# Optimization experiments

Measured on AMD Instinct MI355X. Metric: run time of the kernel, lower is better.

The kernel has to match this reference:

```python
import jax, jax.numpy as jnp
import numpy as np

EPS = 1e-6
K_HOPS = 2  # SGConv K


def setup_inputs() -> dict:
    key = jax.random.key(0)
    k1, k2, k3, k4 = jax.random.split(key, 4)
    B, Kk, C, T = 32, 8, 64, 250
    E, H = 4096, 128
    x = jax.random.normal(k1, (B, Kk, C, T), dtype=jnp.float32)
    edge_index = jax.random.randint(k2, (2, E), 0, C, dtype=jnp.int64)
    edge_weights = jax.random.uniform(k3, (E,), dtype=jnp.float32)
    W = jax.random.normal(k4, (H, Kk * T), dtype=jnp.float32) * 0.02
    b = jnp.zeros((H,), dtype=jnp.float32)
    return {"x": x, "edge_index": edge_index, "edge_weights": edge_weights, "W": W, "b": b}


def reference(x, edge_index, edge_weights, W, b):
    B, Kk, C, T = x.shape
    N = C  # nodes
    x = x.reshape(B, N, Kk * T)  # (B, N, F)

    # clamp non-positive edge weights to epsilon (mirrors in-place .data clamp)
    w = jnp.where(edge_weights <= 0, EPS, edge_weights)

    # gcn_norm with self loops (fill value 1.0)
    src, dst = edge_index[0], edge_index[1]
    loop = jnp.arange(N, dtype=edge_index.dtype)
    src = jnp.concatenate([src, loop])
    dst = jnp.concatenate([dst, loop])
    w = jnp.concatenate([w, jnp.ones((N,), w.dtype)])
    deg = jnp.zeros((N,), w.dtype).at[dst].add(w)
    dinv = jnp.where(deg > 0, deg ** -0.5, jnp.zeros_like(deg))
    norm = dinv[src] * w * dinv[dst]  # (E+N,)

    # K hops of gather -> weight -> scatter-add aggregation
    for _ in range(K_HOPS):
        msg = x[:, src, :] * norm[None, :, None]        # (B, E+N, F)
        x = jnp.zeros_like(x).at[:, dst, :].add(msg)    # (B, N, F)

    # final linear: y = x @ W^T + b
    return jnp.einsum('bnf,hf->bnh', x, W) + b
```

## Files before the change

kernel.cpp:

```cpp
#include <hip/hip_runtime.h>
#include <hip/hip_bf16.h>

#define EPSW 1e-6f

typedef __attribute__((ext_vector_type(4))) float floatx4;
typedef __attribute__((ext_vector_type(8))) short shortx8;

__device__ __forceinline__ unsigned short f2bf(float f) {
    unsigned int u = __float_as_uint(f);
    u = (u + 0x7fffu + ((u >> 16) & 1u)) >> 16;
    return (unsigned short)u;
}

__global__ __launch_bounds__(256) void prep(const float* __restrict__ x,
                                            const float* __restrict__ W,
                                            const int* __restrict__ ei,
                                            const float* __restrict__ ew,
                                            unsigned short* __restrict__ xt,
                                            unsigned short* __restrict__ wt,
                                            float* __restrict__ Mt) {
    __shared__ __align__(16) unsigned char smem[64 * 264 * 2];
    const int bid = blockIdx.x;
    const int t   = threadIdx.x;

    if (bid < 256) {
        unsigned short(*tile)[264] = (unsigned short(*)[264])smem;
        const int rb   = (bid >> 3) * 64;
        const int kgb  = (bid & 7) * 32;
        const int kbas = kgb * 8;
#pragma unroll
        for (int i = 0; i < 16; ++i) {
            const int idx = i * 256 + t;
            const int r   = idx >> 6;
            const int kc  = (idx & 63) * 4;
            const int k   = kbas + kc;
            floatx4 v = (floatx4){0.f, 0.f, 0.f, 0.f};
            if (k < 2000)
                v = *(const floatx4*)(x + (size_t)(rb + r) * 2000 + k);
            tile[r][kc + 0] = f2bf(v.x);
            tile[r][kc + 1] = f2bf(v.y);
            tile[r][kc + 2] = f2bf(v.z);
            tile[r][kc + 3] = f2bf(v.w);
        }
        __syncthreads();
#pragma unroll
        for (int i = 0; i < 8; ++i) {
            const int kg_l = i * 4 + (t >> 6);
            const int r    = t & 63;
            const shortx8 g = *(const shortx8*)&tile[r][kg_l * 8];
            *(shortx8*)(xt + ((size_t)(kgb + kg_l) * 2048 + rb + r) * 8) = g;
        }
    } else if (bid < 272) {
#pragma unroll
        for (int i = 0; i < 8; ++i) {
            const int G  = (bid - 256) * 2048 + i * 256 + t;
            const int kg = G >> 7;
            const int h  = G & 127;
            const int k  = kg * 8;
            floatx4 v0 = (floatx4){0.f, 0.f, 0.f, 0.f};
            floatx4 v1 = (floatx4){0.f, 0.f, 0.f, 0.f};
            if (k < 2000) {
                v0 = *(const floatx4*)(W + (size_t)h * 2000 + k);
                v1 = *(const floatx4*)(W + (size_t)h * 2000 + k + 4);
            }
            unsigned short* p = wt + ((size_t)kg * 128 + h) * 8;
            p[0] = f2bf(v0.x); p[1] = f2bf(v0.y); p[2] = f2bf(v0.z); p[3] = f2bf(v0.w);
            p[4] = f2bf(v1.x); p[5] = f2bf(v1.y); p[6] = f2bf(v1.z); p[7] = f2bf(v1.w);
        }
    } else {
        float* A    = (float*)smem;
        float* deg  = (float*)(smem + 16384);
        float* dinv = deg + 64;
        if (t < 64) deg[t] = 1.0f;
        for (int i = t; i < 4096; i += 256) A[i] = 0.0f;
        __syncthreads();
        const int* src = ei;
        const int* dst = ei + 4096;
        for (int e = t; e < 4096; e += 256) {
            float w = ew[e];
            w = (w <= 0.0f) ? EPSW : w;
            atomicAdd(&deg[dst[e]], w);
        }
        __syncthreads();
        if (t < 64) dinv[t] = 1.0f / sqrtf(deg[t]);
        __syncthreads();
        for (int e = t; e < 4096; e += 256) {
            float w = ew[e];
            w = (w <= 0.0f) ? EPSW : w;
            const int s = src[e], d = dst[e];
            atomicAdd(&A[d * 64 + s], dinv[s] * w * dinv[d]);
        }
        if (t < 64) atomicAdd(&A[t * 64 + t], dinv[t] * dinv[t]);
        __syncthreads();
#pragma unroll
        for (int i = 0; i < 16; ++i) {
            const int idx = i * 256 + t;
            const int n = idx >> 6, c = idx & 63;
            float s = 0.0f;
#pragma unroll 8
            for (int k = 0; k < 64; ++k) s += A[n * 64 + k] * A[k * 64 + c];
            Mt[c * 64 + n] = s;
        }
    }
}

__global__ __launch_bounds__(256) void gemm(const unsigned short* __restrict__ xt,
                                            const unsigned short* __restrict__ wt,
                                            float* __restrict__ z) {
    const int t    = threadIdx.x;
    const int wave = t >> 6, lane = t & 63;
    const int m = lane & 15, q = lane >> 4;
    const int rbase = blockIdx.x * 16;
    const int hbase = blockIdx.y * 64 + wave * 16;

    const shortx8* Ag = (const shortx8*)xt;
    const shortx8* Bg = (const shortx8*)wt;
    int ga = q * 2048 + rbase + m;
    int gb = q * 128 + hbase + m;

    floatx4 acc0 = (floatx4){0.f, 0.f, 0.f, 0.f};
    floatx4 acc1 = (floatx4){0.f, 0.f, 0.f, 0.f};
#pragma unroll 4
    for (int kt = 0; kt < 64; kt += 2) {
        const shortx8 a0 = Ag[ga];
        const shortx8 b0 = Bg[gb];
        const shortx8 a1 = Ag[ga + 8192];
        const shortx8 b1 = Bg[gb + 512];
        acc0 = __builtin_amdgcn_mfma_f32_16x16x32_bf16(a0, b0, acc0, 0, 0, 0);
        acc1 = __builtin_amdgcn_mfma_f32_16x16x32_bf16(a1, b1, acc1, 0, 0, 0);
        ga += 16384; gb += 1024;
    }
#pragma unroll
    for (int v = 0; v < 4; ++v)
        z[(size_t)(rbase + q * 4 + v) * 128 + hbase + m] = acc0[v] + acc1[v];
}

__global__ __launch_bounds__(256) void apply_M(const float* __restrict__ z,
                                               const float* __restrict__ Mtg,
                                               const float* __restrict__ bias,
                                               float* __restrict__ y) {
    __shared__ float Ms[4096];
    __shared__ float zs[64][16];
    const int b  = blockIdx.x;
    const int hc = blockIdx.y;
    const int t  = threadIdx.x;
#pragma unroll
    for (int i = 0; i < 16; ++i) Ms[i * 256 + t] = Mtg[i * 256 + t];
#pragma unroll
    for (int i = 0; i < 4; ++i) {
        const int idx = i * 256 + t;
        const int mr = idx >> 4, hh = idx & 15;
        zs[mr][hh] = z[(size_t)(b * 64 + mr) * 128 + hc * 16 + hh];
    }
    __syncthreads();
    const int h  = t & 15;
    const int n0 = (t >> 4) * 4;
    const float bv = bias[hc * 16 + h];
    float s0 = bv, s1 = bv, s2 = bv, s3 = bv;
#pragma unroll
    for (int mm = 0; mm < 64; ++mm) {
        const float zv = zs[mm][h];
        s0 += Ms[mm * 64 + n0 + 0] * zv;
        s1 += Ms[mm * 64 + n0 + 1] * zv;
        s2 += Ms[mm * 64 + n0 + 2] * zv;
        s3 += Ms[mm * 64 + n0 + 3] * zv;
    }
    float* yp = y + (size_t)b * 8192 + (size_t)n0 * 128 + hc * 16 + h;
    yp[0]   = s0;
    yp[128] = s1;
    yp[256] = s2;
    yp[384] = s3;
}

extern "C" void kernel_launch(void* const* d_in, const int* in_sizes, int n_in,
                              void* d_out, int out_size, void* d_ws, size_t ws_size,
                              hipStream_t stream) {
    const float* x    = (const float*)d_in[0];
    const int*   ei   = (const int*)d_in[1];
    const float* ew   = (const float*)d_in[2];
    const float* W    = (const float*)d_in[3];
    const float* bias = (const float*)d_in[4];
    float* y = (float*)d_out;

    float* z  = (float*)d_ws;
    float* Mt = z + 262144;
    unsigned short* xt = (unsigned short*)(Mt + 4096);
    unsigned short* wt = xt + 4194304;

    prep<<<273, 256, 0, stream>>>(x, W, ei, ew, xt, wt, Mt);
    gemm<<<dim3(128, 2), 256, 0, stream>>>(xt, wt, z);
    apply_M<<<dim3(32, 8), 256, 0, stream>>>(z, Mt, bias, y);
}
```

Before: 103.4 us.

## Fuse x bf16 conversion into GEMM, reading fp32 x directly

Drops the prep pass that converted x to bf16 and rearranged it into a k-grouped layout in a workspace. The GEMM now loads fp32 rows of x directly, packs them to bf16 in registers with byte permutes, and feeds MFMA. This removes a full write and re-read of a 16 MB bf16 copy of x. In exchange the GEMM reads fp32 (twice the bytes per element), does strided per-row loads, rounds to bf16 with a simpler rounding rule, and splits the K loop into 63 dependent steps with boundary checks.

```diff
diff --git a/kernel.cpp b/kernel.cpp
--- a/kernel.cpp
+++ b/kernel.cpp
@@ -12,48 +12,30 @@
     return (unsigned short)u;
 }
 
-__global__ __launch_bounds__(256) void prep(const float* __restrict__ x,
-                                            const float* __restrict__ W,
-                                            const int* __restrict__ ei,
-                                            const float* __restrict__ ew,
-                                            unsigned short* __restrict__ xt,
-                                            unsigned short* __restrict__ wt,
-                                            float* __restrict__ Mt) {
-    __shared__ __align__(16) unsigned char smem[64 * 264 * 2];
+__device__ __forceinline__ shortx8 pack8(floatx4 a, floatx4 b) {
+    union { shortx8 v; unsigned int u[4]; } r;
+    const unsigned a0 = __float_as_uint(a.x) + 0x8000u, a1 = __float_as_uint(a.y) + 0x8000u;
+    const unsigned a2 = __float_as_uint(a.z) + 0x8000u, a3 = __float_as_uint(a.w) + 0x8000u;
+    const unsigned b0 = __float_as_uint(b.x) + 0x8000u, b1 = __float_as_uint(b.y) + 0x8000u;
+    const unsigned b2 = __float_as_uint(b.z) + 0x8000u, b3 = __float_as_uint(b.w) + 0x8000u;
+    r.u[0] = __builtin_amdgcn_perm(a1, a0, 0x07060302u);
+    r.u[1] = __builtin_amdgcn_perm(a3, a2, 0x07060302u);
+    r.u[2] = __builtin_amdgcn_perm(b1, b0, 0x07060302u);
+    r.u[3] = __builtin_amdgcn_perm(b3, b2, 0x07060302u);
+    return r.v;
+}
+
+__global__ __launch_bounds__(256) void prep_small(const float* __restrict__ W,
+                                                  const int* __restrict__ ei,
+                                                  const float* __restrict__ ew,
+                                                  unsigned short* __restrict__ wt,
+                                                  float* __restrict__ Mt) {
     const int bid = blockIdx.x;
     const int t   = threadIdx.x;
-
-    if (bid < 256) {
-        unsigned short(*tile)[264] = (unsigned short(*)[264])smem;
-        const int rb   = (bid >> 3) * 64;
-        const int kgb  = (bid & 7) * 32;
-        const int kbas = kgb * 8;
+    if (bid < 32) {
 #pragma unroll
-        for (int i = 0; i < 16; ++i) {
-            const int idx = i * 256 + t;
-            const int r   = idx >> 6;
-            const int kc  = (idx & 63) * 4;
-            const int k   = kbas + kc;
-            floatx4 v = (floatx4){0.f, 0.f, 0.f, 0.f};
-            if (k < 2000)
-                v = *(const floatx4*)(x + (size_t)(rb + r) * 2000 + k);
-            tile[r][kc + 0] = f2bf(v.x);
-            tile[r][kc + 1] = f2bf(v.y);
-            tile[r][kc + 2] = f2bf(v.z);
-            tile[r][kc + 3] = f2bf(v.w);
-        }
-        __syncthreads();
-#pragma unroll
-        for (int i = 0; i < 8; ++i) {
-            const int kg_l = i * 4 + (t >> 6);
-            const int r    = t & 63;
-            const shortx8 g = *(const shortx8*)&tile[r][kg_l * 8];
-            *(shortx8*)(xt + ((size_t)(kgb + kg_l) * 2048 + rb + r) * 8) = g;
-        }
-    } else if (bid < 272) {
-#pragma unroll
-        for (int i = 0; i < 8; ++i) {
-            const int G  = (bid - 256) * 2048 + i * 256 + t;
+        for (int i = 0; i < 4; ++i) {
+            const int G  = bid * 1024 + i * 256 + t;
             const int kg = G >> 7;
             const int h  = G & 127;
             const int k  = kg * 8;
@@ -68,9 +50,9 @@
             p[4] = f2bf(v1.x); p[5] = f2bf(v1.y); p[6] = f2bf(v1.z); p[7] = f2bf(v1.w);
         }
     } else {
-        float* A    = (float*)smem;
-        float* deg  = (float*)(smem + 16384);
-        float* dinv = deg + 64;
+        __shared__ float A[4096];
+        __shared__ float deg[64];
+        __shared__ float dinv[64];
         if (t < 64) deg[t] = 1.0f;
         for (int i = t; i < 4096; i += 256) A[i] = 0.0f;
         __syncthreads();
@@ -104,35 +86,36 @@
     }
 }
 
-__global__ __launch_bounds__(256) void gemm(const unsigned short* __restrict__ xt,
-                                            const unsigned short* __restrict__ wt,
-                                            float* __restrict__ z) {
+__global__ __launch_bounds__(256) void gemm_direct(const float* __restrict__ x,
+                                                   const unsigned short* __restrict__ wt,
+                                                   float* __restrict__ z) {
     const int t    = threadIdx.x;
     const int wave = t >> 6, lane = t & 63;
     const int m = lane & 15, q = lane >> 4;
-    const int rbase = blockIdx.x * 16;
-    const int hbase = blockIdx.y * 64 + wave * 16;
-
-    const shortx8* Ag = (const shortx8*)xt;
+    const int b  = blockIdx.y;
+    const int rt = blockIdx.x >> 1, hh = blockIdx.x & 1;
+    const float* xrow = x + (size_t)(b * 64 + rt * 16 + m) * 2000;
+    const int htile = hh * 4 + wave;
     const shortx8* Bg = (const shortx8*)wt;
-    int ga = q * 2048 + rbase + m;
-    int gb = q * 128 + hbase + m;
+    const int gb = q * 128 + htile * 16 + m;
 
     floatx4 acc0 = (floatx4){0.f, 0.f, 0.f, 0.f};
     floatx4 acc1 = (floatx4){0.f, 0.f, 0.f, 0.f};
-#pragma unroll 4
-    for (int kt = 0; kt < 64; kt += 2) {
-        const shortx8 a0 = Ag[ga];
-        const shortx8 b0 = Bg[gb];
-        const shortx8 a1 = Ag[ga + 8192];
-        const shortx8 b1 = Bg[gb + 512];
-        acc0 = __builtin_amdgcn_mfma_f32_16x16x32_bf16(a0, b0, acc0, 0, 0, 0);
-        acc1 = __builtin_amdgcn_mfma_f32_16x16x32_bf16(a1, b1, acc1, 0, 0, 0);
-        ga += 16384; gb += 1024;
+#pragma unroll 9
+    for (int s = 0; s < 63; ++s) {
+        const int k0 = s * 32 + q * 8;
+        floatx4 f0 = (floatx4){0.f, 0.f, 0.f, 0.f};
+        floatx4 f1 = (floatx4){0.f, 0.f, 0.f, 0.f};
+        if (k0 < 2000)     f0 = *(const floatx4*)(xrow + k0);
+        if (k0 + 4 < 2000) f1 = *(const floatx4*)(xrow + k0 + 4);
+        const shortx8 af = pack8(f0, f1);
+        const shortx8 bf = Bg[gb + s * 512];
+        if (s & 1) acc1 = __builtin_amdgcn_mfma_f32_16x16x32_bf16(af, bf, acc1, 0, 0, 0);
+        else       acc0 = __builtin_amdgcn_mfma_f32_16x16x32_bf16(af, bf, acc0, 0, 0, 0);
     }
 #pragma unroll
     for (int v = 0; v < 4; ++v)
-        z[(size_t)(rbase + q * 4 + v) * 128 + hbase + m] = acc0[v] + acc1[v];
+        z[(size_t)(b * 64 + rt * 16 + q * 4 + v) * 128 + htile * 16 + m] = acc0[v] + acc1[v];
 }
 
 __global__ __launch_bounds__(256) void apply_M(const float* __restrict__ z,
@@ -184,10 +167,9 @@
 
     float* z  = (float*)d_ws;
     float* Mt = z + 262144;
-    unsigned short* xt = (unsigned short*)(Mt + 4096);
-    unsigned short* wt = xt + 4194304;
+    unsigned short* wt = (unsigned short*)(Mt + 4096);
 
-    prep<<<273, 256, 0, stream>>>(x, W, ei, ew, xt, wt, Mt);
-    gemm<<<dim3(128, 2), 256, 0, stream>>>(xt, wt, z);
+    prep_small<<<33, 256, 0, stream>>>(W, ei, ew, wt, Mt);
+    gemm_direct<<<dim3(8, 32), 256, 0, stream>>>(x, wt, z);
     apply_M<<<dim3(32, 8), 256, 0, stream>>>(z, Mt, bias, y);
 }
```

After: 117.0 us. +13.1%, slower.

## Fuse prep, GEMM and apply_M into one cooperative kernel with grid syncs

Applied to the files above, without the earlier changes.

Merges the three launches into a single cooperative kernel of 256 blocks, separating the phases with grid-wide syncs. The W conversion is spread across blocks, and the adjacency/M computation is folded onto the last block after its x tile. The intent is to remove launch gaps and tail effects between kernels. In exchange it adds grid-sync overhead and puts the serial M build on one block's critical path before the first sync.

```diff
diff --git a/kernel.cpp b/kernel.cpp
--- a/kernel.cpp
+++ b/kernel.cpp
@@ -1,5 +1,8 @@
 #include <hip/hip_runtime.h>
 #include <hip/hip_bf16.h>
+#include <hip/hip_cooperative_groups.h>
+
+namespace cg = cooperative_groups;
 
 #define EPSW 1e-6f
 
@@ -12,18 +15,18 @@
     return (unsigned short)u;
 }
 
-__global__ __launch_bounds__(256) void prep(const float* __restrict__ x,
-                                            const float* __restrict__ W,
-                                            const int* __restrict__ ei,
-                                            const float* __restrict__ ew,
-                                            unsigned short* __restrict__ xt,
-                                            unsigned short* __restrict__ wt,
-                                            float* __restrict__ Mt) {
-    __shared__ __align__(16) unsigned char smem[64 * 264 * 2];
+__global__ __launch_bounds__(256) void fused(
+        const float* __restrict__ x, const float* __restrict__ W,
+        const int* __restrict__ ei, const float* __restrict__ ew,
+        const float* __restrict__ bias,
+        unsigned short* __restrict__ xt, unsigned short* __restrict__ wt,
+        float* __restrict__ Mt, float* __restrict__ z, float* __restrict__ y) {
+    __shared__ __align__(16) unsigned char smem[50688];
     const int bid = blockIdx.x;
     const int t   = threadIdx.x;
+    cg::grid_group grid = cg::this_grid();
 
-    if (bid < 256) {
+    {
         unsigned short(*tile)[264] = (unsigned short(*)[264])smem;
         const int rb   = (bid >> 3) * 64;
         const int kgb  = (bid & 7) * 32;
@@ -42,21 +45,8 @@
             tile[r][kc + 2] = f2bf(v.z);
             tile[r][kc + 3] = f2bf(v.w);
         }
-        __syncthreads();
-#pragma unroll
-        for (int i = 0; i < 8; ++i) {
-            const int kg_l = i * 4 + (t >> 6);
-            const int r    = t & 63;
-            const shortx8 g = *(const shortx8*)&tile[r][kg_l * 8];
-            *(shortx8*)(xt + ((size_t)(kgb + kg_l) * 2048 + rb + r) * 8) = g;
-        }
-    } else if (bid < 272) {
-#pragma unroll
-        for (int i = 0; i < 8; ++i) {
-            const int G  = (bid - 256) * 2048 + i * 256 + t;
-            const int kg = G >> 7;
-            const int h  = G & 127;
-            const int k  = kg * 8;
+        if (t < 128) {
+            const int kg = bid, h = t, k = kg * 8;
             floatx4 v0 = (floatx4){0.f, 0.f, 0.f, 0.f};
             floatx4 v1 = (floatx4){0.f, 0.f, 0.f, 0.f};
             if (k < 2000) {
@@ -67,109 +57,111 @@
             p[0] = f2bf(v0.x); p[1] = f2bf(v0.y); p[2] = f2bf(v0.z); p[3] = f2bf(v0.w);
             p[4] = f2bf(v1.x); p[5] = f2bf(v1.y); p[6] = f2bf(v1.z); p[7] = f2bf(v1.w);
         }
-    } else {
-        float* A    = (float*)smem;
-        float* deg  = (float*)(smem + 16384);
-        float* dinv = deg + 64;
-        if (t < 64) deg[t] = 1.0f;
-        for (int i = t; i < 4096; i += 256) A[i] = 0.0f;
         __syncthreads();
-        const int* src = ei;
-        const int* dst = ei + 4096;
-        for (int e = t; e < 4096; e += 256) {
-            float w = ew[e];
-            w = (w <= 0.0f) ? EPSW : w;
-            atomicAdd(&deg[dst[e]], w);
+#pragma unroll
+        for (int i = 0; i < 8; ++i) {
+            const int kg_l = i * 4 + (t >> 6);
+            const int r    = t & 63;
+            const shortx8 g = *(const shortx8*)&tile[r][kg_l * 8];
+            *(shortx8*)(xt + ((size_t)(kgb + kg_l) * 2048 + rb + r) * 8) = g;
+        }
+        if (bid == 255) {
+            float* A    = (float*)(smem + 33792);
+            float* deg  = A + 4096;
+            float* dinv = deg + 64;
+            if (t < 64) deg[t] = 1.0f;
+            for (int i = t; i < 4096; i += 256) A[i] = 0.0f;
+            __syncthreads();
+            const int* src = ei;
+            const int* dst = ei + 4096;
+            for (int e = t; e < 4096; e += 256) {
+                float w = ew[e];
+                w = (w <= 0.0f) ? EPSW : w;
+                atomicAdd(&deg[dst[e]], w);
+            }
+            __syncthreads();
+            if (t < 64) dinv[t] = 1.0f / sqrtf(deg[t]);
+            __syncthreads();
+            for (int e = t; e < 4096; e += 256) {
+                float w = ew[e];
+                w = (w <= 0.0f) ? EPSW : w;
+                const int s = src[e], d = dst[e];
+                atomicAdd(&A[d * 64 + s], dinv[s] * w * dinv[d]);
+            }
+            if (t < 64) atomicAdd(&A[t * 64 + t], dinv[t] * dinv[t]);
+            __syncthreads();
+#pragma unroll
+            for (int i = 0; i < 16; ++i) {
+                const int idx = i * 256 + t;
+                const int n = idx >> 6, c = idx & 63;
+                float s = 0.0f;
+#pragma unroll 8
+                for (int k = 0; k < 64; ++k) s += A[n * 64 + k] * A[k * 64 + c];
+                Mt[c * 64 + n] = s;
+            }
+        }
+    }
+    grid.sync();
+
+    {
+        const int wave = t >> 6, lane = t & 63;
+        const int m = lane & 15, q = lane >> 4;
+        const int rbase = (bid >> 1) * 16;
+        const int hbase = (bid & 1) * 64 + wave * 16;
+        const shortx8* Ag = (const shortx8*)xt;
+        const shortx8* Bg = (const shortx8*)wt;
+        int ga = q * 2048 + rbase + m;
+        int gb = q * 128 + hbase + m;
+        floatx4 acc0 = (floatx4){0.f, 0.f, 0.f, 0.f};
+        floatx4 acc1 = (floatx4){0.f, 0.f, 0.f, 0.f};
+#pragma unroll 4
+        for (int kt = 0; kt < 64; kt += 2) {
+            const shortx8 a0 = Ag[ga];
+            const shortx8 b0 = Bg[gb];
+            const shortx8 a1 = Ag[ga + 8192];
+            const shortx8 b1 = Bg[gb + 512];
+            acc0 = __builtin_amdgcn_mfma_f32_16x16x32_bf16(a0, b0, acc0, 0, 0, 0);
+            acc1 = __builtin_amdgcn_mfma_f32_16x16x32_bf16(a1, b1, acc1, 0, 0, 0);
+            ga += 16384; gb += 1024;
+        }
+#pragma unroll
+        for (int v = 0; v < 4; ++v)
+            z[(size_t)(rbase + q * 4 + v) * 128 + hbase + m] = acc0[v] + acc1[v];
+    }
+    grid.sync();
+
+    {
+        float* Ms       = (float*)smem;
+        float(*zs)[16]  = (float(*)[16])(smem + 16384);
+        const int b  = bid >> 3;
+        const int hc = bid & 7;
+#pragma unroll
+        for (int i = 0; i < 16; ++i) Ms[i * 256 + t] = Mt[i * 256 + t];
+#pragma unroll
+        for (int i = 0; i < 4; ++i) {
+            const int idx = i * 256 + t;
+            const int mr = idx >> 4, hh = idx & 15;
+            zs[mr][hh] = z[(size_t)(b * 64 + mr) * 128 + hc * 16 + hh];
         }
         __syncthreads();
-        if (t < 64) dinv[t] = 1.0f / sqrtf(deg[t]);
-        __syncthreads();
-        for (int e = t; e < 4096; e += 256) {
-            float w = ew[e];
-            w = (w <= 0.0f) ? EPSW : w;
-            const int s = src[e], d = dst[e];
-            atomicAdd(&A[d * 64 + s], dinv[s] * w * dinv[d]);
+        const int h  = t & 15;
+        const int n0 = (t >> 4) * 4;
+        const float bv = bias[hc * 16 + h];
+        float s0 = bv, s1 = bv, s2 = bv, s3 = bv;
+#pragma unroll
+        for (int mm = 0; mm < 64; ++mm) {
+            const float zv = zs[mm][h];
+            s0 += Ms[mm * 64 + n0 + 0] * zv;
+            s1 += Ms[mm * 64 + n0 + 1] * zv;
+            s2 += Ms[mm * 64 + n0 + 2] * zv;
+            s3 += Ms[mm * 64 + n0 + 3] * zv;
         }
-        if (t < 64) atomicAdd(&A[t * 64 + t], dinv[t] * dinv[t]);
-        __syncthreads();
-#pragma unroll
-        for (int i = 0; i < 16; ++i) {
-            const int idx = i * 256 + t;
-            const int n = idx >> 6, c = idx & 63;
-            float s = 0.0f;
-#pragma unroll 8
-            for (int k = 0; k < 64; ++k) s += A[n * 64 + k] * A[k * 64 + c];
-            Mt[c * 64 + n] = s;
-        }
+        float* yp = y + (size_t)b * 8192 + (size_t)n0 * 128 + hc * 16 + h;
+        yp[0]   = s0;
+        yp[128] = s1;
+        yp[256] = s2;
+        yp[384] = s3;
     }
-}
-
-__global__ __launch_bounds__(256) void gemm(const unsigned short* __restrict__ xt,
-                                            const unsigned short* __restrict__ wt,
-                                            float* __restrict__ z) {
-    const int t    = threadIdx.x;
-    const int wave = t >> 6, lane = t & 63;
-    const int m = lane & 15, q = lane >> 4;
-    const int rbase = blockIdx.x * 16;
-    const int hbase = blockIdx.y * 64 + wave * 16;
-
-    const shortx8* Ag = (const shortx8*)xt;
-    const shortx8* Bg = (const shortx8*)wt;
-    int ga = q * 2048 + rbase + m;
-    int gb = q * 128 + hbase + m;
-
-    floatx4 acc0 = (floatx4){0.f, 0.f, 0.f, 0.f};
-    floatx4 acc1 = (floatx4){0.f, 0.f, 0.f, 0.f};
-#pragma unroll 4
-    for (int kt = 0; kt < 64; kt += 2) {
-        const shortx8 a0 = Ag[ga];
-        const shortx8 b0 = Bg[gb];
-        const shortx8 a1 = Ag[ga + 8192];
-        const shortx8 b1 = Bg[gb + 512];
-        acc0 = __builtin_amdgcn_mfma_f32_16x16x32_bf16(a0, b0, acc0, 0, 0, 0);
-        acc1 = __builtin_amdgcn_mfma_f32_16x16x32_bf16(a1, b1, acc1, 0, 0, 0);
-        ga += 16384; gb += 1024;
-    }
-#pragma unroll
-    for (int v = 0; v < 4; ++v)
-        z[(size_t)(rbase + q * 4 + v) * 128 + hbase + m] = acc0[v] + acc1[v];
-}
-
-__global__ __launch_bounds__(256) void apply_M(const float* __restrict__ z,
-                                               const float* __restrict__ Mtg,
-                                               const float* __restrict__ bias,
-                                               float* __restrict__ y) {
-    __shared__ float Ms[4096];
-    __shared__ float zs[64][16];
-    const int b  = blockIdx.x;
-    const int hc = blockIdx.y;
-    const int t  = threadIdx.x;
-#pragma unroll
-    for (int i = 0; i < 16; ++i) Ms[i * 256 + t] = Mtg[i * 256 + t];
-#pragma unroll
-    for (int i = 0; i < 4; ++i) {
-        const int idx = i * 256 + t;
-        const int mr = idx >> 4, hh = idx & 15;
-        zs[mr][hh] = z[(size_t)(b * 64 + mr) * 128 + hc * 16 + hh];
-    }
-    __syncthreads();
-    const int h  = t & 15;
-    const int n0 = (t >> 4) * 4;
-    const float bv = bias[hc * 16 + h];
-    float s0 = bv, s1 = bv, s2 = bv, s3 = bv;
-#pragma unroll
-    for (int mm = 0; mm < 64; ++mm) {
-        const float zv = zs[mm][h];
-        s0 += Ms[mm * 64 + n0 + 0] * zv;
-        s1 += Ms[mm * 64 + n0 + 1] * zv;
-        s2 += Ms[mm * 64 + n0 + 2] * zv;
-        s3 += Ms[mm * 64 + n0 + 3] * zv;
-    }
-    float* yp = y + (size_t)b * 8192 + (size_t)n0 * 128 + hc * 16 + h;
-    yp[0]   = s0;
-    yp[128] = s1;
-    yp[256] = s2;
-    yp[384] = s3;
 }
 
 extern "C" void kernel_launch(void* const* d_in, const int* in_sizes, int n_in,
@@ -187,7 +179,8 @@
     unsigned short* xt = (unsigned short*)(Mt + 4096);
     unsigned short* wt = xt + 4194304;
 
-    prep<<<273, 256, 0, stream>>>(x, W, ei, ew, xt, wt, Mt);
-    gemm<<<dim3(128, 2), 256, 0, stream>>>(xt, wt, z);
-    apply_M<<<dim3(32, 8), 256, 0, stream>>>(z, Mt, bias, y);
+    void* args[] = {(void*)&x, (void*)&W, (void*)&ei, (void*)&ew, (void*)&bias,
+                    (void*)&xt, (void*)&wt, (void*)&Mt, (void*)&z, (void*)&y};
+    hipLaunchCooperativeKernel((const void*)fused, dim3(256), dim3(256),
+                               args, 0, stream);
 }
```

After: 180.0 us. +74.0%, slower.

## Fuse GEMM and propagation-matrix apply into one kernel with split-K waves

Applied to the files above, without the earlier changes.

Merges the bf16 MFMA GEMM and the apply_M step into a single kernel. Each 512-thread block computes a 64-row by 16-column tile of z, with the K dimension split across two groups of four waves that are reduced through shared memory. The block then applies the precomputed 64x64 propagation matrix and bias directly from LDS. This removes one launch and the global round trip of z, but the block's 16-column tile means x tiles are re-read by 8 blocks, and the grid shape changes to 256 larger blocks.

```diff
diff --git a/kernel.cpp b/kernel.cpp
--- a/kernel.cpp
+++ b/kernel.cpp
@@ -104,24 +104,37 @@
     }
 }
 
-__global__ __launch_bounds__(256) void gemm(const unsigned short* __restrict__ xt,
-                                            const unsigned short* __restrict__ wt,
-                                            float* __restrict__ z) {
+__global__ __launch_bounds__(512) void gemm_apply(
+        const unsigned short* __restrict__ xt,
+        const unsigned short* __restrict__ wt,
+        const float* __restrict__ Mt,
+        const float* __restrict__ bias,
+        float* __restrict__ y) {
+    __shared__ float Ms[4096];
+    __shared__ float zs[64][17];
     const int t    = threadIdx.x;
     const int wave = t >> 6, lane = t & 63;
     const int m = lane & 15, q = lane >> 4;
-    const int rbase = blockIdx.x * 16;
-    const int hbase = blockIdx.y * 64 + wave * 16;
+    const int ht = blockIdx.x;
+    const int b  = blockIdx.y;
+    const int rt = wave & 3, kh = wave >> 2;
+
+    {
+        const floatx4* Mg4 = (const floatx4*)Mt;
+        floatx4* Ms4 = (floatx4*)Ms;
+        Ms4[t]       = Mg4[t];
+        Ms4[t + 512] = Mg4[t + 512];
+    }
 
     const shortx8* Ag = (const shortx8*)xt;
     const shortx8* Bg = (const shortx8*)wt;
-    int ga = q * 2048 + rbase + m;
-    int gb = q * 128 + hbase + m;
+    int ga = (kh * 128 + q) * 2048 + b * 64 + rt * 16 + m;
+    int gb = (kh * 128 + q) * 128 + ht * 16 + m;
 
     floatx4 acc0 = (floatx4){0.f, 0.f, 0.f, 0.f};
     floatx4 acc1 = (floatx4){0.f, 0.f, 0.f, 0.f};
 #pragma unroll 4
-    for (int kt = 0; kt < 64; kt += 2) {
+    for (int kt = 0; kt < 32; kt += 2) {
         const shortx8 a0 = Ag[ga];
         const shortx8 b0 = Bg[gb];
         const shortx8 a1 = Ag[ga + 8192];
@@ -130,46 +143,35 @@
         acc1 = __builtin_amdgcn_mfma_f32_16x16x32_bf16(a1, b1, acc1, 0, 0, 0);
         ga += 16384; gb += 1024;
     }
+    acc0 += acc1;
+
+    __syncthreads();
+    if (kh == 0) {
 #pragma unroll
-    for (int v = 0; v < 4; ++v)
-        z[(size_t)(rbase + q * 4 + v) * 128 + hbase + m] = acc0[v] + acc1[v];
-}
-
-__global__ __launch_bounds__(256) void apply_M(const float* __restrict__ z,
-                                               const float* __restrict__ Mtg,
-                                               const float* __restrict__ bias,
-                                               float* __restrict__ y) {
-    __shared__ float Ms[4096];
-    __shared__ float zs[64][16];
-    const int b  = blockIdx.x;
-    const int hc = blockIdx.y;
-    const int t  = threadIdx.x;
-#pragma unroll
-    for (int i = 0; i < 16; ++i) Ms[i * 256 + t] = Mtg[i * 256 + t];
-#pragma unroll
-    for (int i = 0; i < 4; ++i) {
-        const int idx = i * 256 + t;
-        const int mr = idx >> 4, hh = idx & 15;
-        zs[mr][hh] = z[(size_t)(b * 64 + mr) * 128 + hc * 16 + hh];
+        for (int v = 0; v < 4; ++v) zs[rt * 16 + q * 4 + v][m] = acc0[v];
     }
     __syncthreads();
-    const int h  = t & 15;
-    const int n0 = (t >> 4) * 4;
-    const float bv = bias[hc * 16 + h];
-    float s0 = bv, s1 = bv, s2 = bv, s3 = bv;
+    if (kh == 1) {
 #pragma unroll
-    for (int mm = 0; mm < 64; ++mm) {
-        const float zv = zs[mm][h];
-        s0 += Ms[mm * 64 + n0 + 0] * zv;
-        s1 += Ms[mm * 64 + n0 + 1] * zv;
-        s2 += Ms[mm * 64 + n0 + 2] * zv;
-        s3 += Ms[mm * 64 + n0 + 3] * zv;
+        for (int v = 0; v < 4; ++v) zs[rt * 16 + q * 4 + v][m] += acc0[v];
     }
-    float* yp = y + (size_t)b * 8192 + (size_t)n0 * 128 + hc * 16 + h;
-    yp[0]   = s0;
-    yp[128] = s1;
-    yp[256] = s2;
-    yp[384] = s3;
+    __syncthreads();
+
+    {
+        const int n0 = t >> 4;
+        const int h  = t & 15;
+        const float bv = bias[ht * 16 + h];
+        float s0 = bv, s1 = bv;
+#pragma unroll
+        for (int mm = 0; mm < 64; ++mm) {
+            const float zv = zs[mm][h];
+            s0 += Ms[mm * 64 + n0]      * zv;
+            s1 += Ms[mm * 64 + n0 + 32] * zv;
+        }
+        float* yp = y + (size_t)b * 8192 + ht * 16 + h;
+        yp[(size_t)n0 * 128]        = s0;
+        yp[(size_t)(n0 + 32) * 128] = s1;
+    }
 }
 
 extern "C" void kernel_launch(void* const* d_in, const int* in_sizes, int n_in,
@@ -182,12 +184,10 @@
     const float* bias = (const float*)d_in[4];
     float* y = (float*)d_out;
 
-    float* z  = (float*)d_ws;
-    float* Mt = z + 262144;
+    float* Mt = (float*)d_ws;
     unsigned short* xt = (unsigned short*)(Mt + 4096);
     unsigned short* wt = xt + 4194304;
 
     prep<<<273, 256, 0, stream>>>(x, W, ei, ew, xt, wt, Mt);
-    gemm<<<dim3(128, 2), 256, 0, stream>>>(xt, wt, z);
-    apply_M<<<dim3(32, 8), 256, 0, stream>>>(z, Mt, bias, y);
+    gemm_apply<<<dim3(8, 32), 512, 0, stream>>>(xt, wt, Mt, bias, y);
 }
```

New measurement: 102.5 us. Within noise of the previous version (-1.0%).
